# Kernel tuning notes

Measured on AMD Instinct MI355X. Metric: run time of the kernel, lower is better.

Reference implementation:

```python
import jax, jax.numpy as jnp
import numpy as np

NUM_ITERATIONS = 3


def squash(t, axis=-1):
    # scale * t / sqrt(||t||^2), scale = ||t||^2 / (1 + ||t||^2)
    sq = jnp.sum(t * t, axis=axis, keepdims=True)
    return (sq / (1.0 + sq)) * t / jnp.sqrt(sq)


def setup_inputs() -> dict:
    key = jax.random.key(0)
    k1, k2 = jax.random.split(key)
    x = jax.random.normal(k1, (256, 1152, 8), dtype=jnp.float32)
    route_weights = jax.random.normal(k2, (10, 1152, 8, 16), dtype=jnp.float32)
    return {"x": x, "route_weights": route_weights}


def reference(x, route_weights):
    # priors[c,b,n,1,o] = x[b,n,:] @ route_weights[c,n,:,:]
    priors = jnp.einsum('bni,cnio->cbno', x, route_weights)[:, :, :, None, :]
    logits = jnp.zeros_like(priors)
    outputs = None
    for i in range(NUM_ITERATIONS):
        probs = jax.nn.softmax(logits, axis=2)  # softmax over route nodes (dim=2), as in source
        outputs = squash(jnp.sum(probs * priors, axis=2, keepdims=True))  # [c,b,1,1,o]
        if i != NUM_ITERATIONS - 1:
            delta = jnp.sum(priors * outputs, axis=-1, keepdims=True)  # [c,b,n,1,1]
            logits = logits + delta  # broadcasts over last dim
    return outputs
```

## Files before the change

kernel.cpp:

```cpp
#include <hip/hip_runtime.h>

#define NCAP 10
#define NB   256
#define NN   1152
#define KI   8
#define NO   16
#define NT   1024
#define NWV  16
#define TB   2
#define NITER 3

__global__ __launch_bounds__(NT) void capsule_kernel(
    const float* __restrict__ x,
    const float* __restrict__ w,
    float* __restrict__ out)
{
    __shared__ unsigned s_pr[NO/2][TB][NN];
    __shared__ float s_red2[NWV][TB][NO];
    __shared__ float s_ls[NWV][TB];
    __shared__ float s_v[TB][NO];

    const int t    = threadIdx.x;
    const int wv   = t >> 6;
    const int lane = t & 63;
    const int j    = t & 3;
    const int g    = t >> 2;

    const int bid = blockIdx.x;
    const int swz = (bid & 7) * (NCAP * (NB / TB) / 8) + (bid >> 3);
    const int c   = swz / (NB / TB);
    const int b0  = (swz % (NB / TB)) * TB;

    const int bl0 = lane & 1, bl1 = (lane >> 1) & 1,
              bl2 = (lane >> 2) & 1, bl3 = (lane >> 3) & 1;

    float bs[TB][4] = {{0.f,0.f,0.f,0.f},{0.f,0.f,0.f,0.f}};

    auto build_round = [&](int n) {
        const float4* wp = reinterpret_cast<const float4*>(
            w + ((size_t)c * NN + n) * (KI * NO));
        float xs[TB][KI];
        #pragma unroll
        for (int tb = 0; tb < TB; ++tb) {
            const float4* xp = reinterpret_cast<const float4*>(
                x + ((size_t)(b0 + tb) * NN + n) * KI);
            float4 a = xp[0], b = xp[1];
            xs[tb][0]=a.x; xs[tb][1]=a.y; xs[tb][2]=a.z; xs[tb][3]=a.w;
            xs[tb][4]=b.x; xs[tb][5]=b.y; xs[tb][6]=b.z; xs[tb][7]=b.w;
        }
        float acc[TB][4] = {{0.f,0.f,0.f,0.f},{0.f,0.f,0.f,0.f}};
        #pragma unroll
        for (int i = 0; i < KI; ++i) {
            float4 wq = wp[i * 4 + j];
            #pragma unroll
            for (int tb = 0; tb < TB; ++tb) {
                acc[tb][0] = fmaf(xs[tb][i], wq.x, acc[tb][0]);
                acc[tb][1] = fmaf(xs[tb][i], wq.y, acc[tb][1]);
                acc[tb][2] = fmaf(xs[tb][i], wq.z, acc[tb][2]);
                acc[tb][3] = fmaf(xs[tb][i], wq.w, acc[tb][3]);
            }
        }
        #pragma unroll
        for (int tb = 0; tb < TB; ++tb) {
            bs[tb][0] += acc[tb][0]; bs[tb][1] += acc[tb][1];
            bs[tb][2] += acc[tb][2]; bs[tb][3] += acc[tb][3];
            unsigned p0, p1;
            asm("v_cvt_pk_bf16_f32 %0, %1, %2"
                : "=v"(p0) : "v"(acc[tb][0]), "v"(acc[tb][1]));
            asm("v_cvt_pk_bf16_f32 %0, %1, %2"
                : "=v"(p1) : "v"(acc[tb][2]), "v"(acc[tb][3]));
            s_pr[2*j+0][tb][n] = p0;
            s_pr[2*j+1][tb][n] = p1;
        }
    };
    #pragma unroll 1
    for (int r = 0; r < 4; ++r) build_round(r * 256 + g);
    if (g < 128) build_round(1024 + g);

    #pragma unroll
    for (int tb = 0; tb < TB; ++tb)
        #pragma unroll
        for (int k = 0; k < 4; ++k) {
            float s = bs[tb][k];
            s += __shfl_xor(s, 4);  s += __shfl_xor(s, 8);
            s += __shfl_xor(s, 16); s += __shfl_xor(s, 32);
            bs[tb][k] = s;
        }
    if (lane < 4) {
        #pragma unroll
        for (int tb = 0; tb < TB; ++tb) {
            s_red2[wv][tb][4*lane+0] = bs[tb][0];
            s_red2[wv][tb][4*lane+1] = bs[tb][1];
            s_red2[wv][tb][4*lane+2] = bs[tb][2];
            s_red2[wv][tb][4*lane+3] = bs[tb][3];
        }
    }
    __syncthreads();

    auto finalize = [&](int iter) {
        if (t < TB * NO) {
            const int tb = t >> 4, oc = t & 15;
            float acc = 0.f, lt = 0.f;
            #pragma unroll
            for (int w2 = 0; w2 < NWV; ++w2) {
                acc += s_red2[w2][tb][oc];
                if (iter > 0) lt += s_ls[w2][tb];
            }
            if (iter == 0) lt = (float)NN;
            float s_o = acc / lt;
            float sq = s_o * s_o;
            sq += __shfl_xor(sq, 1); sq += __shfl_xor(sq, 2);
            sq += __shfl_xor(sq, 4); sq += __shfl_xor(sq, 8);
            float scale = sq / ((1.f + sq) * sqrtf(sq));
            float vo = s_o * scale;
            s_v[tb][oc] = vo;
            if (iter == NITER - 1)
                out[((size_t)c * NB + b0 + tb) * NO + oc] = vo;
        }
    };

    float logit[2][TB] = {{0.f,0.f},{0.f,0.f}};

    auto routing_pass = [&]() {
        #pragma unroll
        for (int tb = 0; tb < TB; ++tb) {
            float vv[NO];
            {
                const float4* vp = reinterpret_cast<const float4*>(&s_v[tb][0]);
                float4 a = vp[0], b = vp[1], cc = vp[2], d4 = vp[3];
                vv[0]=a.x;  vv[1]=a.y;  vv[2]=a.z;  vv[3]=a.w;
                vv[4]=b.x;  vv[5]=b.y;  vv[6]=b.z;  vv[7]=b.w;
                vv[8]=cc.x; vv[9]=cc.y; vv[10]=cc.z; vv[11]=cc.w;
                vv[12]=d4.x; vv[13]=d4.y; vv[14]=d4.z; vv[15]=d4.w;
            }
            float sp[NO];
            #pragma unroll
            for (int o = 0; o < NO; ++o) sp[o] = 0.f;
            float lse = 0.f;
            #pragma unroll
            for (int rr = 0; rr < 2; ++rr) {
                if (rr == 1 && t >= 128) continue;
                const int n = rr * 1024 + t;
                unsigned u[8];
                #pragma unroll
                for (int op = 0; op < 8; ++op) u[op] = s_pr[op][tb][n];
                float d = 0.f;
                #pragma unroll
                for (int op = 0; op < 8; ++op) {
                    float lo = __uint_as_float(u[op] << 16);
                    float hi = __uint_as_float(u[op] & 0xffff0000u);
                    d = fmaf(lo, vv[2*op+0], d);
                    d = fmaf(hi, vv[2*op+1], d);
                }
                logit[rr][tb] += d;
                float e = __expf(logit[rr][tb]);
                lse += e;
                #pragma unroll
                for (int op = 0; op < 8; ++op) {
                    float lo = __uint_as_float(u[op] << 16);
                    float hi = __uint_as_float(u[op] & 0xffff0000u);
                    sp[2*op+0] = fmaf(e, lo, sp[2*op+0]);
                    sp[2*op+1] = fmaf(e, hi, sp[2*op+1]);
                }
            }
            float s = lse;
            s += __shfl_xor(s, 1);  s += __shfl_xor(s, 2);
            s += __shfl_xor(s, 4);  s += __shfl_xor(s, 8);
            s += __shfl_xor(s, 16); s += __shfl_xor(s, 32);
            if (lane == 0) s_ls[wv][tb] = s;
            float g8[8];
            #pragma unroll
            for (int r = 0; r < 8; ++r) {
                float keep = bl0 ? sp[2*r+1] : sp[2*r];
                float send = bl0 ? sp[2*r]   : sp[2*r+1];
                g8[r] = keep + __shfl_xor(send, 1);
            }
            float g4[4];
            #pragma unroll
            for (int r = 0; r < 4; ++r) {
                float keep = bl1 ? g8[2*r+1] : g8[2*r];
                float send = bl1 ? g8[2*r]   : g8[2*r+1];
                g4[r] = keep + __shfl_xor(send, 2);
            }
            float g2[2];
            #pragma unroll
            for (int r = 0; r < 2; ++r) {
                float keep = bl2 ? g4[2*r+1] : g4[2*r];
                float send = bl2 ? g4[2*r]   : g4[2*r+1];
                g2[r] = keep + __shfl_xor(send, 4);
            }
            float g1;
            {
                float keep = bl3 ? g2[1] : g2[0];
                float send = bl3 ? g2[0] : g2[1];
                g1 = keep + __shfl_xor(send, 8);
            }
            g1 += __shfl_xor(g1, 16);
            g1 += __shfl_xor(g1, 32);
            if (lane < NO) s_red2[wv][tb][lane] = g1;
        }
    };

    finalize(0);
    __syncthreads();
    routing_pass();
    __syncthreads();
    finalize(1);
    __syncthreads();
    routing_pass();
    __syncthreads();
    finalize(2);
}

extern "C" void kernel_launch(void* const* d_in, const int* in_sizes, int n_in,
                              void* d_out, int out_size, void* d_ws, size_t ws_size,
                              hipStream_t stream) {
    const float* x = (const float*)d_in[0];
    const float* w = (const float*)d_in[1];
    float* out = (float*)d_out;
    capsule_kernel<<<dim3(NCAP * (NB / TB)), dim3(NT), 0, stream>>>(x, w, out);
}
```

Baseline: 59.93 us.

## Finalize redundantly in every wave, swizzle priors LDS, hoist weight loads

Every wave now performs the finalize reduction and squash itself and writes its own copy of the output vector into per-wave shared storage. The routing pass reads that copy, so one thread subset no longer does serial work while all others wait. The bf16 prior stores in LDS are XOR-swizzled by output-pair index to avoid bank conflicts, and the eight weight float4 loads are issued up front before the FMAs to raise memory-level parallelism. The dot product is split into two accumulator chains. The redundant finalize repeats the reduction in all 16 waves, which adds shared-memory reads.

```diff
diff --git a/kernel.cpp b/kernel.cpp
--- a/kernel.cpp
+++ b/kernel.cpp
@@ -16,9 +16,9 @@
     float* __restrict__ out)
 {
     __shared__ unsigned s_pr[NO/2][TB][NN];
-    __shared__ float s_red2[NWV][TB][NO];
-    __shared__ float s_ls[NWV][TB];
-    __shared__ float s_v[TB][NO];
+    __shared__ float s_part[NWV][TB][NO];
+    __shared__ float s_lsum[NWV][TB];
+    __shared__ float s_vw[NWV][TB][NO];
 
     const int t    = threadIdx.x;
     const int wv   = t >> 6;
@@ -37,8 +37,6 @@
     float bs[TB][4] = {{0.f,0.f,0.f,0.f},{0.f,0.f,0.f,0.f}};
 
     auto build_round = [&](int n) {
-        const float4* wp = reinterpret_cast<const float4*>(
-            w + ((size_t)c * NN + n) * (KI * NO));
         float xs[TB][KI];
         #pragma unroll
         for (int tb = 0; tb < TB; ++tb) {
@@ -48,18 +46,23 @@
             xs[tb][0]=a.x; xs[tb][1]=a.y; xs[tb][2]=a.z; xs[tb][3]=a.w;
             xs[tb][4]=b.x; xs[tb][5]=b.y; xs[tb][6]=b.z; xs[tb][7]=b.w;
         }
+        const float4* wp = reinterpret_cast<const float4*>(
+            w + ((size_t)c * NN + n) * (KI * NO));
+        float4 wq[8];
+        #pragma unroll
+        for (int i = 0; i < KI; ++i) wq[i] = wp[i * 4 + j];
         float acc[TB][4] = {{0.f,0.f,0.f,0.f},{0.f,0.f,0.f,0.f}};
         #pragma unroll
         for (int i = 0; i < KI; ++i) {
-            float4 wq = wp[i * 4 + j];
             #pragma unroll
             for (int tb = 0; tb < TB; ++tb) {
-                acc[tb][0] = fmaf(xs[tb][i], wq.x, acc[tb][0]);
-                acc[tb][1] = fmaf(xs[tb][i], wq.y, acc[tb][1]);
-                acc[tb][2] = fmaf(xs[tb][i], wq.z, acc[tb][2]);
-                acc[tb][3] = fmaf(xs[tb][i], wq.w, acc[tb][3]);
-            }
-        }
+                acc[tb][0] = fmaf(xs[tb][i], wq[i].x, acc[tb][0]);
+                acc[tb][1] = fmaf(xs[tb][i], wq[i].y, acc[tb][1]);
+                acc[tb][2] = fmaf(xs[tb][i], wq[i].z, acc[tb][2]);
+                acc[tb][3] = fmaf(xs[tb][i], wq[i].w, acc[tb][3]);
+            }
+        }
+        const int o0 = 2 * j, o1 = 2 * j + 1;
         #pragma unroll
         for (int tb = 0; tb < TB; ++tb) {
             bs[tb][0] += acc[tb][0]; bs[tb][1] += acc[tb][1];
@@ -69,8 +72,8 @@
                 : "=v"(p0) : "v"(acc[tb][0]), "v"(acc[tb][1]));
             asm("v_cvt_pk_bf16_f32 %0, %1, %2"
                 : "=v"(p1) : "v"(acc[tb][2]), "v"(acc[tb][3]));
-            s_pr[2*j+0][tb][n] = p0;
-            s_pr[2*j+1][tb][n] = p1;
+            s_pr[o0][tb][n ^ (o0 << 2)] = p0;
+            s_pr[o1][tb][n ^ (o1 << 2)] = p1;
         }
     };
     #pragma unroll 1
@@ -89,34 +92,32 @@
     if (lane < 4) {
         #pragma unroll
         for (int tb = 0; tb < TB; ++tb) {
-            s_red2[wv][tb][4*lane+0] = bs[tb][0];
-            s_red2[wv][tb][4*lane+1] = bs[tb][1];
-            s_red2[wv][tb][4*lane+2] = bs[tb][2];
-            s_red2[wv][tb][4*lane+3] = bs[tb][3];
+            s_part[wv][tb][4*lane+0] = bs[tb][0];
+            s_part[wv][tb][4*lane+1] = bs[tb][1];
+            s_part[wv][tb][4*lane+2] = bs[tb][2];
+            s_part[wv][tb][4*lane+3] = bs[tb][3];
         }
     }
-    __syncthreads();
 
     auto finalize = [&](int iter) {
-        if (t < TB * NO) {
-            const int tb = t >> 4, oc = t & 15;
-            float acc = 0.f, lt = 0.f;
-            #pragma unroll
-            for (int w2 = 0; w2 < NWV; ++w2) {
-                acc += s_red2[w2][tb][oc];
-                if (iter > 0) lt += s_ls[w2][tb];
-            }
-            if (iter == 0) lt = (float)NN;
-            float s_o = acc / lt;
-            float sq = s_o * s_o;
-            sq += __shfl_xor(sq, 1); sq += __shfl_xor(sq, 2);
-            sq += __shfl_xor(sq, 4); sq += __shfl_xor(sq, 8);
-            float scale = sq / ((1.f + sq) * sqrtf(sq));
-            float vo = s_o * scale;
-            s_v[tb][oc] = vo;
-            if (iter == NITER - 1)
-                out[((size_t)c * NB + b0 + tb) * NO + oc] = vo;
-        }
+        const int tb2 = (lane >> 4) & 1;
+        const int oc  = lane & 15;
+        float acc = 0.f, lt = 0.f;
+        #pragma unroll
+        for (int w2 = 0; w2 < NWV; ++w2) {
+            acc += s_part[w2][tb2][oc];
+            if (iter > 0) lt += s_lsum[w2][tb2];
+        }
+        if (iter == 0) lt = (float)NN;
+        float s_o = acc / lt;
+        float sq = s_o * s_o;
+        sq += __shfl_xor(sq, 1); sq += __shfl_xor(sq, 2);
+        sq += __shfl_xor(sq, 4); sq += __shfl_xor(sq, 8);
+        float scale = sq / ((1.f + sq) * sqrtf(sq));
+        float vo = s_o * scale;
+        if (lane < 32) s_vw[wv][tb2][oc] = vo;
+        if (iter == NITER - 1 && wv == 0 && lane < 32)
+            out[((size_t)c * NB + b0 + tb2) * NO + oc] = vo;
     };
 
     float logit[2][TB] = {{0.f,0.f},{0.f,0.f}};
@@ -125,14 +126,8 @@
         #pragma unroll
         for (int tb = 0; tb < TB; ++tb) {
             float vv[NO];
-            {
-                const float4* vp = reinterpret_cast<const float4*>(&s_v[tb][0]);
-                float4 a = vp[0], b = vp[1], cc = vp[2], d4 = vp[3];
-                vv[0]=a.x;  vv[1]=a.y;  vv[2]=a.z;  vv[3]=a.w;
-                vv[4]=b.x;  vv[5]=b.y;  vv[6]=b.z;  vv[7]=b.w;
-                vv[8]=cc.x; vv[9]=cc.y; vv[10]=cc.z; vv[11]=cc.w;
-                vv[12]=d4.x; vv[13]=d4.y; vv[14]=d4.z; vv[15]=d4.w;
-            }
+            #pragma unroll
+            for (int o = 0; o < NO; ++o) vv[o] = s_vw[wv][tb][o];
             float sp[NO];
             #pragma unroll
             for (int o = 0; o < NO; ++o) sp[o] = 0.f;
@@ -141,33 +136,30 @@
             for (int rr = 0; rr < 2; ++rr) {
                 if (rr == 1 && t >= 128) continue;
                 const int n = rr * 1024 + t;
-                unsigned u[8];
-                #pragma unroll
-                for (int op = 0; op < 8; ++op) u[op] = s_pr[op][tb][n];
-                float d = 0.f;
+                float row[NO];
                 #pragma unroll
                 for (int op = 0; op < 8; ++op) {
-                    float lo = __uint_as_float(u[op] << 16);
-                    float hi = __uint_as_float(u[op] & 0xffff0000u);
-                    d = fmaf(lo, vv[2*op+0], d);
-                    d = fmaf(hi, vv[2*op+1], d);
+                    unsigned u = s_pr[op][tb][n ^ (op << 2)];
+                    row[2*op+0] = __uint_as_float(u << 16);
+                    row[2*op+1] = __uint_as_float(u & 0xffff0000u);
                 }
-                logit[rr][tb] += d;
+                float d0 = 0.f, d1 = 0.f;
+                #pragma unroll
+                for (int o = 0; o < 8; ++o) {
+                    d0 = fmaf(row[o],     vv[o],     d0);
+                    d1 = fmaf(row[o + 8], vv[o + 8], d1);
+                }
+                logit[rr][tb] += d0 + d1;
                 float e = __expf(logit[rr][tb]);
                 lse += e;
                 #pragma unroll
-                for (int op = 0; op < 8; ++op) {
-                    float lo = __uint_as_float(u[op] << 16);
-                    float hi = __uint_as_float(u[op] & 0xffff0000u);
-                    sp[2*op+0] = fmaf(e, lo, sp[2*op+0]);
-                    sp[2*op+1] = fmaf(e, hi, sp[2*op+1]);
-                }
+                for (int o = 0; o < NO; ++o) sp[o] = fmaf(e, row[o], sp[o]);
             }
             float s = lse;
             s += __shfl_xor(s, 1);  s += __shfl_xor(s, 2);
             s += __shfl_xor(s, 4);  s += __shfl_xor(s, 8);
             s += __shfl_xor(s, 16); s += __shfl_xor(s, 32);
-            if (lane == 0) s_ls[wv][tb] = s;
+            if (lane == 0) s_lsum[wv][tb] = s;
             float g8[8];
             #pragma unroll
             for (int r = 0; r < 8; ++r) {
@@ -197,10 +189,11 @@
             }
             g1 += __shfl_xor(g1, 16);
             g1 += __shfl_xor(g1, 32);
-            if (lane < NO) s_red2[wv][tb][lane] = g1;
+            if (lane < NO) s_part[wv][tb][lane] = g1;
         }
     };
 
+    __syncthreads();
     finalize(0);
     __syncthreads();
     routing_pass();
```

After: 90.44 us. 1.51x slower.
